# Kernel optimization log

Measured on AMD Instinct MI355X. Metric: run time of the kernel, lower is better.

The kernel has to match this reference:

```python
import jax, jax.numpy as jnp
import numpy as np

N_NODES = 100000
N_EDGES = 600000
N_GRAPHS = 2000
H = 128
L = 3
EPS = 1e-5


def layer_norm(x, g, b):
    m = jnp.mean(x, axis=-1, keepdims=True)
    v = jnp.mean((x - m) ** 2, axis=-1, keepdims=True)
    return (x - m) / jnp.sqrt(v + EPS) * g + b


def setup_inputs() -> dict:
    key = jax.random.key(0)
    ks = jax.random.split(key, 32)
    s = 0.05
    d = {}
    d['atom_features'] = jax.random.normal(ks[0], (N_NODES, 4), jnp.float32)
    d['edge_index'] = jax.random.randint(ks[1], (2, N_EDGES), 0, N_NODES, jnp.int32)
    d['edge_attr'] = jax.random.uniform(ks[2], (N_EDGES, 1), jnp.float32)
    d['batch'] = jnp.sort(jax.random.randint(ks[3], (N_NODES,), 0, N_GRAPHS, jnp.int32))
    # atom encoder
    d['enc_w'] = jax.random.normal(ks[4], (4, H)) * s
    d['enc_b'] = jnp.zeros((H,))
    d['enc_ln_g'] = jnp.ones((H,))
    d['enc_ln_b'] = jnp.zeros((H,))
    # stacked per-layer MPNN params (L layers)
    d['msg_w1'] = jax.random.normal(ks[5], (L, 2 * H + 1, 2 * H)) * s
    d['msg_b1'] = jnp.zeros((L, 2 * H))
    d['msg_w2'] = jax.random.normal(ks[6], (L, 2 * H, H)) * s
    d['msg_b2'] = jnp.zeros((L, H))
    d['gru_wih'] = jax.random.normal(ks[7], (L, 3 * H, H)) * s
    d['gru_whh'] = jax.random.normal(ks[8], (L, 3 * H, H)) * s
    d['gru_bih'] = jnp.zeros((L, 3 * H))
    d['gru_bhh'] = jnp.zeros((L, 3 * H))
    d['ln_g'] = jnp.ones((L, H))
    d['ln_b'] = jnp.zeros((L, H))
    # readout MLP (dropout is eval-mode identity)
    d['ro_w1'] = jax.random.normal(ks[9], (2 * H, H)) * s
    d['ro_b1'] = jnp.zeros((H,))
    d['ro_w2'] = jax.random.normal(ks[10], (H, H // 2)) * s
    d['ro_b2'] = jnp.zeros((H // 2,))
    d['ro_w3'] = jax.random.normal(ks[11], (H // 2, 113)) * s
    d['ro_b3'] = jnp.zeros((113,))
    return d


def _forward(atom_features, edge_attr, enc_w, enc_b, enc_ln_g, enc_ln_b,
             msg_w1, msg_b1, msg_w2, msg_b2, gru_wih, gru_whh, gru_bih, gru_bhh,
             ln_g, ln_b, ro_w1, ro_b1, ro_w2, ro_b2, ro_w3, ro_b3,
             edge_index, batch):
    n = atom_features.shape[0]
    x = layer_norm(jax.nn.relu(atom_features @ enc_w + enc_b), enc_ln_g, enc_ln_b)
    src, dst = edge_index[0], edge_index[1]
    for l in range(L):
        # gather-concat-MLP messages: [E, 2H+1] -> [E, 2H] -> [E, H]
        m = jnp.concatenate([x[src], x[dst], edge_attr], axis=-1)
        m = jax.nn.relu(m @ msg_w1[l] + msg_b1[l]) @ msg_w2[l] + msg_b2[l]
        aggr = jax.ops.segment_sum(m, dst, num_segments=n)  # index_add
        # GRUCell(input=aggr, hidden=x)
        gi = aggr @ gru_wih[l].T + gru_bih[l]
        gh = x @ gru_whh[l].T + gru_bhh[l]
        i_r, i_z, i_n = jnp.split(gi, 3, axis=-1)
        h_r, h_z, h_n = jnp.split(gh, 3, axis=-1)
        r = jax.nn.sigmoid(i_r + h_r)
        z = jax.nn.sigmoid(i_z + h_z)
        nn_ = jnp.tanh(i_n + r * h_n)
        x_new = (1.0 - z) * nn_ + z * x
        x = layer_norm(x + x_new, ln_g[l], ln_b[l])
    # per-graph mean+max pooling
    ones = jnp.ones((n,), x.dtype)
    counts = jax.ops.segment_sum(ones, batch, num_segments=N_GRAPHS)
    mean_pool = jax.ops.segment_sum(x, batch, num_segments=N_GRAPHS) / jnp.maximum(counts, 1.0)[:, None]
    max_pool = jax.ops.segment_max(x, batch, num_segments=N_GRAPHS)
    g = jnp.concatenate([mean_pool, max_pool], axis=-1)  # [B, 2H]
    h1 = jax.nn.relu(g @ ro_w1 + ro_b1)
    h2 = jax.nn.relu(h1 @ ro_w2 + ro_b2)
    return h2 @ ro_w3 + ro_b3  # [B, 113]


def reference(atom_features, edge_index, edge_attr, batch, enc_w, enc_b, enc_ln_g, enc_ln_b,
              msg_w1, msg_b1, msg_w2, msg_b2, gru_wih, gru_whh, gru_bih, gru_bhh,
              ln_g, ln_b, ro_w1, ro_b1, ro_w2, ro_b2, ro_w3, ro_b3):
    return _forward(atom_features, edge_attr, enc_w, enc_b, enc_ln_g, enc_ln_b,
                    msg_w1, msg_b1, msg_w2, msg_b2, gru_wih, gru_whh, gru_bih, gru_bhh,
                    ln_g, ln_b, ro_w1, ro_b1, ro_w2, ro_b2, ro_w3, ro_b3,
                    edge_index, batch)
```

## Files before the change

### kernel.cpp

```cpp
#include <hip/hip_runtime.h>
#include <hip/hip_bf16.h>
#include <math.h>

#define NN 100000
#define NE_TOT 600000
#define NG 2000
#define HD 128
#define NL 3
#define LN_EPS 1e-5f

typedef __attribute__((ext_vector_type(8))) short short8;
typedef __attribute__((ext_vector_type(4))) float f32x4;

__device__ __forceinline__ unsigned short f2bf(float f){
  union { float f; unsigned int u; } x; x.f = f;
  unsigned int r = (x.u + 0x7FFFu + ((x.u >> 16) & 1u)) >> 16;
  return (unsigned short)r;
}
__device__ __forceinline__ float bf2f(unsigned short u){
  union { unsigned int i; float f; } x; x.i = ((unsigned int)u) << 16; return x.f;
}

__device__ __forceinline__ float wave_sum64(float v){
  #pragma unroll
  for (int o = 32; o > 0; o >>= 1) v += __shfl_xor(v, o, 64);
  return v;
}

__global__ __launch_bounds__(256) void k_zero4(float4* p, int n4){
  int i = blockIdx.x * 256 + threadIdx.x;
  if (i < n4) p[i] = make_float4(0.f, 0.f, 0.f, 0.f);
}

__global__ __launch_bounds__(256) void k_hist(const int* __restrict__ ei, int* __restrict__ cnt){
  int e = blockIdx.x * 256 + threadIdx.x;
  if (e < NE_TOT) atomicAdd(&cnt[ei[NE_TOT + e]], 1);
}

__global__ __launch_bounds__(1024) void k_scan1(const int* __restrict__ cnt,
                                                int* __restrict__ loc,
                                                int* __restrict__ bsum){
  __shared__ int w_s[16];
  int t = threadIdx.x, lane = t & 63, wv = t >> 6;
  int g = blockIdx.x * 1024 + t;
  int v = (g < NN) ? cnt[g] : 0;
  int s = v;
  #pragma unroll
  for (int o = 1; o < 64; o <<= 1){
    int u = __shfl_up(s, o, 64);
    if (lane >= o) s += u;
  }
  if (lane == 63) w_s[wv] = s;
  __syncthreads();
  if (t == 0){
    int run = 0;
    #pragma unroll
    for (int i = 0; i < 16; ++i){ int c = w_s[i]; w_s[i] = run; run += c; }
    bsum[blockIdx.x] = run;
  }
  __syncthreads();
  if (g < NN) loc[g] = s - v + w_s[wv];
}

__global__ __launch_bounds__(128) void k_scan2(const int* __restrict__ bsum,
                                               int* __restrict__ bscan){
  __shared__ int w0_s;
  int t = threadIdx.x, lane = t & 63, wv = t >> 6;
  int v = (t < 98) ? bsum[t] : 0;
  int s = v;
  #pragma unroll
  for (int o = 1; o < 64; o <<= 1){
    int u = __shfl_up(s, o, 64);
    if (lane >= o) s += u;
  }
  if (wv == 0 && lane == 63) w0_s = s;
  __syncthreads();
  if (wv == 1) s += w0_s;
  if (t < 98) bscan[t] = s - v;
}

__global__ __launch_bounds__(1024) void k_scan3(const int* __restrict__ loc,
                                                const int* __restrict__ bscan,
                                                int* __restrict__ cur){
  int g = blockIdx.x * 1024 + threadIdx.x;
  if (g < NN) cur[g] = loc[g] + bscan[blockIdx.x];
}

__global__ __launch_bounds__(256) void k_scatter(const int* __restrict__ ei,
    const float* __restrict__ eattr, int* __restrict__ cur,
    int* __restrict__ srcs, int* __restrict__ dsts, float* __restrict__ attrs){
  int e = blockIdx.x * 256 + threadIdx.x;
  if (e >= NE_TOT) return;
  int d = ei[NE_TOT + e];
  int p = atomicAdd(&cur[d], 1);
  srcs[p] = ei[e];
  dsts[p] = d;
  attrs[p] = eattr[e];
}

#define GW_LPL 102400
#define GW_O2  67584
#define GW_O3  84992
__global__ __launch_bounds__(256) void k_gprep(const float* __restrict__ wih,
                                               const float* __restrict__ whh,
                                               unsigned short* __restrict__ gw){
  int idx = blockIdx.x * 256 + threadIdx.x;
  if (idx >= 2 * 3 * 384 * 128) return;
  int which = (idx >= 3 * 384 * 128);
  int i = which ? idx - 3 * 384 * 128 : idx;
  int l = i / 49152;
  int r = i - l * 49152;
  int j = r >> 7, k = r & 127;
  float v = which ? whh[i] : wih[i];
  size_t o;
  if (!which){
    o = (j < 256) ? ((size_t)l * GW_LPL + (size_t)j * 264 + k)
                  : ((size_t)l * GW_LPL + GW_O2 + (size_t)(j - 256) * 136 + k);
  } else {
    o = (j < 256) ? ((size_t)l * GW_LPL + (size_t)j * 264 + 128 + k)
                  : ((size_t)l * GW_LPL + GW_O3 + (size_t)(j - 256) * 136 + k);
  }
  gw[o] = f2bf(v);
}

#define W1N_LS (512 * 136)
__global__ __launch_bounds__(256) void k_mprep(const float* __restrict__ w1,
                                               unsigned short* __restrict__ w1n){
  int idx = blockIdx.x * 256 + threadIdx.x;
  if (idx >= 3 * 512 * 128) return;
  int l = idx / (512 * 128);
  int r = idx - l * (512 * 128);
  int j = r >> 7, k = r & 127;
  const float* wl = w1 + (size_t)l * 257 * 256;
  float v = (j < 256) ? wl[k * 256 + j] : wl[(128 + k) * 256 + (j - 256)];
  w1n[(size_t)l * W1N_LS + j * 136 + k] = f2bf(v);
}

#define W2T_LS (128 * 264)
__global__ __launch_bounds__(256) void k_w2prep(const float* __restrict__ w2,
                                                unsigned short* __restrict__ w2T){
  int idx = blockIdx.x * 256 + threadIdx.x;
  if (idx >= 3 * 128 * 256) return;
  int l = idx >> 15;
  int r = idx & 32767;
  int c = r >> 8, k = r & 255;
  w2T[(size_t)l * W2T_LS + c * 264 + k] = f2bf(w2[(size_t)l * 256 * 128 + k * 128 + c]);
}

__global__ __launch_bounds__(256) void k_enc(const float* __restrict__ af,
    const float* __restrict__ w, const float* __restrict__ b,
    const float* __restrict__ lg, const float* __restrict__ lb,
    unsigned short* __restrict__ xbf){
  int wv = threadIdx.x >> 6, lane = threadIdx.x & 63;
  int n = blockIdx.x * 4 + wv;
  float4 a = *reinterpret_cast<const float4*>(af + (size_t)n * 4);
  int c0 = lane, c1 = lane + 64;
  float v0 = fmaf(a.x, w[c0], fmaf(a.y, w[128 + c0], fmaf(a.z, w[256 + c0], fmaf(a.w, w[384 + c0], b[c0]))));
  float v1 = fmaf(a.x, w[c1], fmaf(a.y, w[128 + c1], fmaf(a.z, w[256 + c1], fmaf(a.w, w[384 + c1], b[c1]))));
  v0 = fmaxf(v0, 0.f); v1 = fmaxf(v1, 0.f);
  float m = wave_sum64(v0 + v1) * (1.f / 128.f);
  float d0 = v0 - m, d1 = v1 - m;
  float var = wave_sum64(d0 * d0 + d1 * d1) * (1.f / 128.f);
  float rstd = rsqrtf(var + LN_EPS);
  xbf[(size_t)n * HD + c0] = f2bf(d0 * rstd * lg[c0] + lb[c0]);
  xbf[(size_t)n * HD + c1] = f2bf(d1 * rstd * lg[c1] + lb[c1]);
}

__global__ __launch_bounds__(256, 2) void k_ngemm(const unsigned short* __restrict__ xbf,
    const unsigned short* __restrict__ w1n, const float* __restrict__ b1,
    unsigned short* __restrict__ gsd, float* __restrict__ aggr){
  int tid = threadIdx.x, lane = tid & 63, wv = tid >> 6;
  int r16 = lane & 15, kg = lane >> 4;
  {
    int nrow = NN - blockIdx.x * 64; if (nrow > 64) nrow = 64;
    float4* az = (float4*)(aggr + (size_t)blockIdx.x * 64 * HD);
    int n4 = nrow * (HD / 4);
    for (int i = tid; i < n4; i += 256) az[i] = make_float4(0.f, 0.f, 0.f, 0.f);
  }
  int n = blockIdx.x * 64 + wv * 16 + r16;
  int nc = (n < NN) ? n : NN - 1;
  short8 bfr[4];
  #pragma unroll
  for (int k0 = 0; k0 < 4; ++k0)
    bfr[k0] = *reinterpret_cast<const short8*>(xbf + (size_t)nc * HD + k0 * 32 + kg * 8);
  f32x4 acc[32];
  #pragma unroll
  for (int it = 0; it < 32; ++it) acc[it] = (f32x4){0.f, 0.f, 0.f, 0.f};
  #pragma unroll
  for (int it = 0; it < 32; ++it){
    const unsigned short* ap = w1n + (size_t)(it * 16 + r16) * 136 + kg * 8;
    #pragma unroll
    for (int k0 = 0; k0 < 4; ++k0){
      short8 af = *reinterpret_cast<const short8*>(ap + k0 * 32);
      acc[it] = __builtin_amdgcn_mfma_f32_16x16x32_bf16(af, bfr[k0], acc[it], 0, 0, 0);
    }
  }
  if (n < NN){
    #pragma unroll
    for (int it = 0; it < 32; ++it){
      int c0 = it * 16 + kg * 4;
      ushort4 h;
      float v0 = acc[it][0], v1 = acc[it][1], v2 = acc[it][2], v3 = acc[it][3];
      if (c0 >= 256){
        v0 += b1[c0 - 256]; v1 += b1[c0 - 255]; v2 += b1[c0 - 254]; v3 += b1[c0 - 253];
      }
      h.x = f2bf(v0); h.y = f2bf(v1); h.z = f2bf(v2); h.w = f2bf(v3);
      *reinterpret_cast<ushort4*>(gsd + (size_t)n * 512 + c0) = h;
    }
  }
}

#define EBM 64
__global__ __launch_bounds__(256, 4) void k_msg(const unsigned short* __restrict__ gsd,
    const int* __restrict__ srcs, const int* __restrict__ dsts,
    const float* __restrict__ attrs, const float* __restrict__ w1attr,
    const unsigned short* __restrict__ w2T, const float* __restrict__ b2,
    float* __restrict__ aggr){
  __shared__ __align__(16) unsigned char smem[33280];
  unsigned short* h_s = (unsigned short*)smem;
  float* scr = (float*)smem;
  __shared__ float w1a_s[256];
  __shared__ float b2_s[128];
  __shared__ int   dst_s[EBM];
  __shared__ float attr_s[EBM];
  int tid = threadIdx.x;
  int lane = tid & 63, wv = tid >> 6;
  int r16 = lane & 15, kg = lane >> 4;
  int ebase = blockIdx.x * EBM;

  w1a_s[tid] = w1attr[tid & 255];
  if (tid < 128) b2_s[tid] = b2[tid];
  if (tid < EBM){ dst_s[tid] = dsts[ebase + tid]; attr_s[tid] = attrs[ebase + tid]; }
  __syncthreads();

  {
    int e = tid >> 2, q = tid & 3;
    int sn = srcs[ebase + e];
    int dn = dst_s[e];
    float at = attr_s[e];
    const unsigned short* gp = gsd + (size_t)sn * 512;
    const unsigned short* dp = gsd + (size_t)dn * 512 + 256;
    short8 gv[8], dv[8];
    #pragma unroll
    for (int j8 = 0; j8 < 8; ++j8){
      int colb = j8 * 32 + q * 8;
      gv[j8] = *reinterpret_cast<const short8*>(gp + colb);
      dv[j8] = *reinterpret_cast<const short8*>(dp + colb);
    }
    __builtin_amdgcn_sched_barrier(0);
    #pragma unroll
    for (int j8 = 0; j8 < 8; ++j8){
      int colb = j8 * 32 + q * 8;
      unsigned short hh[8];
      #pragma unroll
      for (int i = 0; i < 8; ++i){
        float v = bf2f((unsigned short)gv[j8][i]) + bf2f((unsigned short)dv[j8][i]) + at * w1a_s[colb + i];
        hh[i] = f2bf(fmaxf(v, 0.f));
      }
      int slot = colb >> 3;
      int slotw = (slot & ~7) | ((slot ^ e) & 7);
      *reinterpret_cast<int4*>(&h_s[e * 256 + slotw * 8]) = *reinterpret_cast<int4*>(hh);
    }
  }
  __syncthreads();

  f32x4 acc2[4][2];
  #pragma unroll
  for (int rt = 0; rt < 4; ++rt)
    #pragma unroll
    for (int ct = 0; ct < 2; ++ct)
      acc2[rt][ct] = (f32x4){0.f, 0.f, 0.f, 0.f};
  int cbase2 = wv * 32;
  {
    short8 a[4], bb[2];
    const unsigned short* w2b = w2T + (size_t)(cbase2 + r16) * 264 + kg * 8;
    for (int k0 = 0; k0 < 8; ++k0){
      #pragma unroll
      for (int rt = 0; rt < 4; ++rt){
        int row = rt * 16 + r16;
        int slot = k0 * 4 + kg;
        int slotw = (slot & ~7) | ((slot ^ row) & 7);
        a[rt] = *reinterpret_cast<const short8*>(&h_s[row * 256 + slotw * 8]);
      }
      #pragma unroll
      for (int ct = 0; ct < 2; ++ct)
        bb[ct] = *reinterpret_cast<const short8*>(w2b + ct * 16 * 264 + k0 * 32);
      #pragma unroll
      for (int rt = 0; rt < 4; ++rt)
        #pragma unroll
        for (int ct = 0; ct < 2; ++ct)
          acc2[rt][ct] = __builtin_amdgcn_mfma_f32_16x16x32_bf16(a[rt], bb[ct], acc2[rt][ct], 0, 0, 0);
    }
  }
  __syncthreads();

  #pragma unroll
  for (int ct = 0; ct < 2; ++ct){
    int col = cbase2 + ct * 16 + r16;
    #pragma unroll
    for (int rt = 0; rt < 4; ++rt){
      #pragma unroll
      for (int r = 0; r < 4; ++r){
        int row = rt * 16 + kg * 4 + r;
        scr[row * 130 + col] = acc2[rt][ct][r];
      }
    }
  }
  __syncthreads();

  {
    int c = tid & 127, h = tid >> 7;
    int r0 = h * 32;
    float bias = b2_s[c];
    int pd = dst_s[r0];
    float acc = scr[r0 * 130 + c] + bias;
    #pragma unroll 4
    for (int r = 1; r < 32; ++r){
      int row = r0 + r;
      float v = scr[row * 130 + c] + bias;
      int d = dst_s[row];
      if (d != pd){
        atomicAdd(&aggr[(size_t)pd * HD + c], acc);
        acc = v; pd = d;
      } else {
        acc += v;
      }
    }
    atomicAdd(&aggr[(size_t)pd * HD + c], acc);
  }
}

#define GRB 64
__global__ __launch_bounds__(256, 2) void k_gru(unsigned short* __restrict__ xbf,
    const float* __restrict__ aggr,
    const unsigned short* __restrict__ gw,
    const float* __restrict__ bih, const float* __restrict__ bhh,
    const float* __restrict__ lg, const float* __restrict__ lb){
  __shared__ unsigned short a_s[GRB * 256];
  __shared__ float psum[GRB][2][2];
  int tid = threadIdx.x;
  int lane = tid & 63, wv = tid >> 6;
  int r16 = lane & 15, kg = lane >> 4;
  int rg = wv >> 1, cg = wv & 1;
  int nbase = blockIdx.x * GRB;

  {
    int row = tid >> 2, qc = (tid & 3) * 32;
    int n = nbase + row; if (n >= NN) n = NN - 1;
    const float* ap = aggr + (size_t)n * HD + qc;
    #pragma unroll
    for (int j = 0; j < 8; ++j){
      float4 v = *reinterpret_cast<const float4*>(ap + j * 4);
      ushort4 h;
      h.x = f2bf(v.x); h.y = f2bf(v.y); h.z = f2bf(v.z); h.w = f2bf(v.w);
      int col = qc + j * 4;
      int slot = col >> 3;
      int slotw = (slot & ~7) | ((slot ^ row) & 7);
      *reinterpret_cast<ushort4*>(&a_s[row * 256 + slotw * 8 + (col & 7)]) = h;
    }
  }
  {
    int row = tid >> 2, q = tid & 3;
    int n = nbase + row; if (n >= NN) n = NN - 1;
    const unsigned short* xp = xbf + (size_t)n * HD + q * 32;
    #pragma unroll
    for (int j = 0; j < 4; ++j){
      int4 v = *reinterpret_cast<const int4*>(xp + j * 8);
      int col = 128 + q * 32 + j * 8;
      int slot = col >> 3;
      int slotw = (slot & ~7) | ((slot ^ row) & 7);
      *reinterpret_cast<int4*>(&a_s[row * 256 + slotw * 8]) = v;
    }
  }
  __syncthreads();

  short8 a[2][8];
  #pragma unroll
  for (int rt = 0; rt < 2; ++rt){
    int arow = rg * 32 + rt * 16 + r16;
    #pragma unroll
    for (int k0 = 0; k0 < 8; ++k0){
      int slot = k0 * 4 + kg;
      int slotw = (slot & ~7) | ((slot ^ arow) & 7);
      a[rt][k0] = *reinterpret_cast<const short8*>(&a_s[arow * 256 + slotw * 8]);
    }
  }

  f32x4 accR[2][4], accZ[2][4], accI[2][4], accH[2][4];
  #pragma unroll
  for (int rt = 0; rt < 2; ++rt)
    #pragma unroll
    for (int ct = 0; ct < 4; ++ct){
      accR[rt][ct] = (f32x4){0.f, 0.f, 0.f, 0.f};
      accZ[rt][ct] = (f32x4){0.f, 0.f, 0.f, 0.f};
      accI[rt][ct] = (f32x4){0.f, 0.f, 0.f, 0.f};
      accH[rt][ct] = (f32x4){0.f, 0.f, 0.f, 0.f};
    }

  int jb = cg * 64;
  #pragma unroll
  for (int ct = 0; ct < 4; ++ct){
    const unsigned short* bpR = gw + (size_t)(jb + ct * 16 + r16) * 264 + kg * 8;
    const unsigned short* bpZ = gw + (size_t)(128 + jb + ct * 16 + r16) * 264 + kg * 8;
    #pragma unroll
    for (int k0 = 0; k0 < 8; ++k0){
      short8 bR = *reinterpret_cast<const short8*>(bpR + k0 * 32);
      accR[0][ct] = __builtin_amdgcn_mfma_f32_16x16x32_bf16(a[0][k0], bR, accR[0][ct], 0, 0, 0);
      accR[1][ct] = __builtin_amdgcn_mfma_f32_16x16x32_bf16(a[1][k0], bR, accR[1][ct], 0, 0, 0);
      short8 bZ = *reinterpret_cast<const short8*>(bpZ + k0 * 32);
      accZ[0][ct] = __builtin_amdgcn_mfma_f32_16x16x32_bf16(a[0][k0], bZ, accZ[0][ct], 0, 0, 0);
      accZ[1][ct] = __builtin_amdgcn_mfma_f32_16x16x32_bf16(a[1][k0], bZ, accZ[1][ct], 0, 0, 0);
    }
    const unsigned short* bpI = gw + GW_O2 + (size_t)(jb + ct * 16 + r16) * 136 + kg * 8;
    const unsigned short* bpH = gw + GW_O3 + (size_t)(jb + ct * 16 + r16) * 136 + kg * 8;
    #pragma unroll
    for (int k0 = 0; k0 < 4; ++k0){
      short8 bI = *reinterpret_cast<const short8*>(bpI + k0 * 32);
      accI[0][ct] = __builtin_amdgcn_mfma_f32_16x16x32_bf16(a[0][k0], bI, accI[0][ct], 0, 0, 0);
      accI[1][ct] = __builtin_amdgcn_mfma_f32_16x16x32_bf16(a[1][k0], bI, accI[1][ct], 0, 0, 0);
      short8 bH = *reinterpret_cast<const short8*>(bpH + k0 * 32);
      accH[0][ct] = __builtin_amdgcn_mfma_f32_16x16x32_bf16(a[0][k0 + 4], bH, accH[0][ct], 0, 0, 0);
      accH[1][ct] = __builtin_amdgcn_mfma_f32_16x16x32_bf16(a[1][k0 + 4], bH, accH[1][ct], 0, 0, 0);
    }
  }

  #pragma unroll
  for (int rt = 0; rt < 2; ++rt){
    #pragma unroll
    for (int ct = 0; ct < 4; ++ct){
      int j = jb + ct * 16 + r16;
      float br = bih[j] + bhh[j];
      float bz = bih[j + 128] + bhh[j + 128];
      float bin = bih[j + 256], bhn = bhh[j + 256];
      #pragma unroll
      for (int r = 0; r < 4; ++r){
        int n = nbase + rg * 32 + rt * 16 + kg * 4 + r;
        int nc = (n < NN) ? n : NN - 1;
        float xv = bf2f(xbf[(size_t)nc * HD + j]);
        float rgt = accR[rt][ct][r] + br;  rgt = 1.f / (1.f + __expf(-rgt));
        float zg  = accZ[rt][ct][r] + bz;  zg  = 1.f / (1.f + __expf(-zg));
        float ng  = tanhf(accI[rt][ct][r] + bin + rgt * (accH[rt][ct][r] + bhn));
        accR[rt][ct][r] = xv + (1.f - zg) * ng + zg * xv;
      }
    }
  }

  #pragma unroll
  for (int rt = 0; rt < 2; ++rt){
    #pragma unroll
    for (int r = 0; r < 4; ++r){
      float s = 0.f, q = 0.f;
      #pragma unroll
      for (int ct = 0; ct < 4; ++ct){ float v = accR[rt][ct][r]; s += v; q += v * v; }
      #pragma unroll
      for (int o = 1; o <= 8; o <<= 1){ s += __shfl_xor(s, o, 64); q += __shfl_xor(q, o, 64); }
      if (r16 == 0){
        int l = rg * 32 + rt * 16 + kg * 4 + r;
        psum[l][cg][0] = s;
        psum[l][cg][1] = q;
      }
    }
  }
  __syncthreads();

  #pragma unroll
  for (int rt = 0; rt < 2; ++rt){
    #pragma unroll
    for (int r = 0; r < 4; ++r){
      int l = rg * 32 + rt * 16 + kg * 4 + r;
      float S = psum[l][0][0] + psum[l][1][0];
      float Q = psum[l][0][1] + psum[l][1][1];
      float m = S * (1.f / 128.f);
      float var = Q * (1.f / 128.f) - m * m;
      float rstd = rsqrtf(fmaxf(var, 0.f) + LN_EPS);
      int n = nbase + rg * 32 + rt * 16 + kg * 4 + r;
      if (n < NN){
        #pragma unroll
        for (int ct = 0; ct < 4; ++ct){
          int j = jb + ct * 16 + r16;
          xbf[(size_t)n * HD + j] = f2bf((accR[rt][ct][r] - m) * rstd * lg[j] + lb[j]);
        }
      }
    }
  }
}

__device__ __forceinline__ int lowerb(const int* __restrict__ a, int v){
  int lo = 0, hi = NN;
  while (lo < hi){ int mid = (lo + hi) >> 1; if (a[mid] < v) lo = mid + 1; else hi = mid; }
  return lo;
}

__global__ __launch_bounds__(128) void k_pool(const unsigned short* __restrict__ xbf,
    const int* __restrict__ batch,
    const float* __restrict__ w1, const float* __restrict__ b1,
    const float* __restrict__ w2, const float* __restrict__ b2,
    const float* __restrict__ w3, const float* __restrict__ b3,
    float* __restrict__ out){
  __shared__ float g_s[256];
  __shared__ float h1_s[128];
  __shared__ float h2_s[64];
  int g = blockIdx.x, tid = threadIdx.x;
  int s = lowerb(batch, g), t = lowerb(batch, g + 1);
  float sum = 0.f, mx = -INFINITY;
  for (int n = s; n < t; ++n){
    float v = bf2f(xbf[(size_t)n * HD + tid]);
    sum += v; mx = fmaxf(mx, v);
  }
  int cnt = t - s;
  g_s[tid]       = sum / fmaxf((float)cnt, 1.f);
  g_s[tid + 128] = (cnt > 0) ? mx : -INFINITY;
  __syncthreads();
  float a1 = b1[tid];
  for (int k = 0; k < 256; ++k) a1 = fmaf(g_s[k], w1[k * 128 + tid], a1);
  h1_s[tid] = fmaxf(a1, 0.f);
  __syncthreads();
  if (tid < 64){
    float a2 = b2[tid];
    for (int k = 0; k < 128; ++k) a2 = fmaf(h1_s[k], w2[k * 64 + tid], a2);
    h2_s[tid] = fmaxf(a2, 0.f);
  }
  __syncthreads();
  if (tid < 113){
    float a3 = b3[tid];
    for (int k = 0; k < 64; ++k) a3 = fmaf(h2_s[k], w3[k * 113 + tid], a3);
    out[(size_t)g * 113 + tid] = a3;
  }
}

extern "C" void kernel_launch(void* const* d_in, const int* in_sizes, int n_in,
                              void* d_out, int out_size, void* d_ws, size_t ws_size,
                              hipStream_t stream){
  (void)in_sizes; (void)n_in; (void)out_size; (void)ws_size;
  const float* af     = (const float*)d_in[0];
  const int*   ei     = (const int*)  d_in[1];
  const float* eattr  = (const float*)d_in[2];
  const int*   batch  = (const int*)  d_in[3];
  const float* enc_w  = (const float*)d_in[4];
  const float* enc_b  = (const float*)d_in[5];
  const float* enc_lg = (const float*)d_in[6];
  const float* enc_lb = (const float*)d_in[7];
  const float* mw1    = (const float*)d_in[8];
  const float* mb1    = (const float*)d_in[9];
  const float* mw2    = (const float*)d_in[10];
  const float* mb2    = (const float*)d_in[11];
  const float* gwih   = (const float*)d_in[12];
  const float* gwhh   = (const float*)d_in[13];
  const float* gbih   = (const float*)d_in[14];
  const float* gbhh   = (const float*)d_in[15];
  const float* lng    = (const float*)d_in[16];
  const float* lnb    = (const float*)d_in[17];
  const float* rw1    = (const float*)d_in[18];
  const float* rb1    = (const float*)d_in[19];
  const float* rw2    = (const float*)d_in[20];
  const float* rb2    = (const float*)d_in[21];
  const float* rw3    = (const float*)d_in[22];
  const float* rb3    = (const float*)d_in[23];
  float* out = (float*)d_out;
  char* ws = (char*)d_ws;

  size_t off = 0;
  auto carve = [&](size_t bytes)->char*{
    char* p = ws + off;
    off = (off + bytes + 255) & ~(size_t)255;
    return p;
  };
  unsigned short* xbf  = (unsigned short*)carve((size_t)NN * HD * 2);
  float*          aggr = (float*)         carve((size_t)NN * HD * 4);
  unsigned short* gsd  = (unsigned short*)carve((size_t)NN * 512 * 2);
  unsigned short* gw   = (unsigned short*)carve((size_t)3 * GW_LPL * 2);
  unsigned short* w1n  = (unsigned short*)carve((size_t)3 * W1N_LS * 2);
  unsigned short* w2T  = (unsigned short*)carve((size_t)3 * W2T_LS * 2);
  int*   cnt   = (int*)  carve((size_t)NN * 4);
  int*   cur   = (int*)  carve((size_t)NN * 4);
  int*   loc   = (int*)  carve((size_t)NN * 4);
  int*   bsum  = (int*)  carve((size_t)128 * 4);
  int*   bscan = (int*)  carve((size_t)128 * 4);
  int*   srcs  = (int*)  carve((size_t)NE_TOT * 4);
  int*   dsts  = (int*)  carve((size_t)NE_TOT * 4);
  float* attrs = (float*)carve((size_t)NE_TOT * 4);

  k_zero4<<<(NN / 4 + 255) / 256, 256, 0, stream>>>((float4*)cnt, NN / 4);
  k_hist<<<(NE_TOT + 255) / 256, 256, 0, stream>>>(ei, cnt);
  k_scan1<<<98, 1024, 0, stream>>>(cnt, loc, bsum);
  k_scan2<<<1, 128, 0, stream>>>(bsum, bscan);
  k_scan3<<<98, 1024, 0, stream>>>(loc, bscan, cur);
  k_scatter<<<(NE_TOT + 255) / 256, 256, 0, stream>>>(ei, eattr, cur, srcs, dsts, attrs);
  k_gprep<<<1152, 256, 0, stream>>>(gwih, gwhh, gw);
  k_mprep<<<768, 256, 0, stream>>>(mw1, w1n);
  k_w2prep<<<384, 256, 0, stream>>>(mw2, w2T);
  k_enc<<<NN / 4, 256, 0, stream>>>(af, enc_w, enc_b, enc_lg, enc_lb, xbf);

  for (int l = 0; l < NL; ++l){
    k_ngemm<<<(NN + 63) / 64, 256, 0, stream>>>(xbf,
        w1n + (size_t)l * W1N_LS, mb1 + (size_t)l * 256, gsd, aggr);
    k_msg<<<NE_TOT / EBM, 256, 0, stream>>>(gsd, srcs, dsts, attrs,
        mw1 + (size_t)l * 257 * 256 + 256 * 256,
        w2T + (size_t)l * W2T_LS, mb2 + (size_t)l * 128, aggr);
    k_gru<<<(NN + GRB - 1) / GRB, 256, 0, stream>>>(xbf, aggr,
        gw + (size_t)l * GW_LPL,
        gbih + (size_t)l * 384, gbhh + (size_t)l * 384,
        lng + (size_t)l * HD, lnb + (size_t)l * HD);
  }
  k_pool<<<NG, 128, 0, stream>>>(xbf, batch, rw1, rb1, rw2, rb2, rw3, rb3, out);
}
```

Measured before the change: 1.002 ms.

## Fold message bias into aggr init, retile node GEMM, vectorize bf16 unpack, cheaper tanh

The second message-layer bias is no longer added per edge. It is folded into the aggregation buffer's initial value as in-degree times the bias, using the histogram counts computed earlier. The node GEMM is retiled so each wave covers 32 nodes by 256 output columns and reuses each weight fragment for two node tiles. The message kernel unpacks bf16 pairs from 32-bit words with shifts and masks, and the GRU uses a sigmoid-based tanh. Together these aim to cut per-edge ALU work and weight-load traffic, at the cost of a slight change in floating-point rounding and a tanh that loses accuracy at extreme inputs.

```diff
diff --git a/kernel.cpp b/kernel.cpp
--- a/kernel.cpp
+++ b/kernel.cpp
@@ -19,6 +19,12 @@
 }
 __device__ __forceinline__ float bf2f(unsigned short u){
   union { unsigned int i; float f; } x; x.i = ((unsigned int)u) << 16; return x.f;
+}
+__device__ __forceinline__ float asfloat_u(unsigned int u){
+  union { unsigned int i; float f; } x; x.i = u; return x.f;
+}
+__device__ __forceinline__ unsigned int pack_bf16x2(float lo, float hi){
+  return (unsigned int)f2bf(lo) | ((unsigned int)f2bf(hi) << 16);
 }
 
 __device__ __forceinline__ float wave_sum64(float v){
@@ -168,44 +174,62 @@
 
 __global__ __launch_bounds__(256, 2) void k_ngemm(const unsigned short* __restrict__ xbf,
     const unsigned short* __restrict__ w1n, const float* __restrict__ b1,
-    unsigned short* __restrict__ gsd, float* __restrict__ aggr){
+    unsigned short* __restrict__ gsd, float* __restrict__ aggr,
+    const int* __restrict__ cnt, const float* __restrict__ b2){
   int tid = threadIdx.x, lane = tid & 63, wv = tid >> 6;
   int r16 = lane & 15, kg = lane >> 4;
+  int rg = wv >> 1, cg = wv & 1;
   {
     int nrow = NN - blockIdx.x * 64; if (nrow > 64) nrow = 64;
-    float4* az = (float4*)(aggr + (size_t)blockIdx.x * 64 * HD);
-    int n4 = nrow * (HD / 4);
-    for (int i = tid; i < n4; i += 256) az[i] = make_float4(0.f, 0.f, 0.f, 0.f);
-  }
-  int n = blockIdx.x * 64 + wv * 16 + r16;
-  int nc = (n < NN) ? n : NN - 1;
-  short8 bfr[4];
-  #pragma unroll
-  for (int k0 = 0; k0 < 4; ++k0)
-    bfr[k0] = *reinterpret_cast<const short8*>(xbf + (size_t)nc * HD + k0 * 32 + kg * 8);
-  f32x4 acc[32];
-  #pragma unroll
-  for (int it = 0; it < 32; ++it) acc[it] = (f32x4){0.f, 0.f, 0.f, 0.f};
-  #pragma unroll
-  for (int it = 0; it < 32; ++it){
-    const unsigned short* ap = w1n + (size_t)(it * 16 + r16) * 136 + kg * 8;
+    for (int i = tid; i < nrow * 32; i += 256){
+      int row = i >> 5, c4 = (i & 31) * 4;
+      int n = blockIdx.x * 64 + row;
+      float cv = (float)cnt[n];
+      float4 bb = *reinterpret_cast<const float4*>(b2 + c4);
+      bb.x *= cv; bb.y *= cv; bb.z *= cv; bb.w *= cv;
+      *reinterpret_cast<float4*>(aggr + (size_t)n * HD + c4) = bb;
+    }
+  }
+  int n0 = blockIdx.x * 64 + rg * 32 + r16;
+  int n1 = n0 + 16;
+  int nc0 = (n0 < NN) ? n0 : NN - 1;
+  int nc1 = (n1 < NN) ? n1 : NN - 1;
+  short8 bfr[2][4];
+  #pragma unroll
+  for (int k0 = 0; k0 < 4; ++k0){
+    bfr[0][k0] = *reinterpret_cast<const short8*>(xbf + (size_t)nc0 * HD + k0 * 32 + kg * 8);
+    bfr[1][k0] = *reinterpret_cast<const short8*>(xbf + (size_t)nc1 * HD + k0 * 32 + kg * 8);
+  }
+  f32x4 acc[2][16];
+  #pragma unroll
+  for (int nt = 0; nt < 2; ++nt)
+    #pragma unroll
+    for (int it = 0; it < 16; ++it) acc[nt][it] = (f32x4){0.f, 0.f, 0.f, 0.f};
+  #pragma unroll
+  for (int it = 0; it < 16; ++it){
+    const unsigned short* ap = w1n + (size_t)(cg * 256 + it * 16 + r16) * 136 + kg * 8;
     #pragma unroll
     for (int k0 = 0; k0 < 4; ++k0){
       short8 af = *reinterpret_cast<const short8*>(ap + k0 * 32);
-      acc[it] = __builtin_amdgcn_mfma_f32_16x16x32_bf16(af, bfr[k0], acc[it], 0, 0, 0);
-    }
-  }
-  if (n < NN){
-    #pragma unroll
-    for (int it = 0; it < 32; ++it){
-      int c0 = it * 16 + kg * 4;
-      ushort4 h;
-      float v0 = acc[it][0], v1 = acc[it][1], v2 = acc[it][2], v3 = acc[it][3];
-      if (c0 >= 256){
-        v0 += b1[c0 - 256]; v1 += b1[c0 - 255]; v2 += b1[c0 - 254]; v3 += b1[c0 - 253];
-      }
-      h.x = f2bf(v0); h.y = f2bf(v1); h.z = f2bf(v2); h.w = f2bf(v3);
-      *reinterpret_cast<ushort4*>(gsd + (size_t)n * 512 + c0) = h;
+      acc[0][it] = __builtin_amdgcn_mfma_f32_16x16x32_bf16(af, bfr[0][k0], acc[0][it], 0, 0, 0);
+      acc[1][it] = __builtin_amdgcn_mfma_f32_16x16x32_bf16(af, bfr[1][k0], acc[1][it], 0, 0, 0);
+    }
+  }
+  #pragma unroll
+  for (int nt = 0; nt < 2; ++nt){
+    int n = blockIdx.x * 64 + rg * 32 + nt * 16 + r16;
+    if (n < NN){
+      #pragma unroll
+      for (int it = 0; it < 16; ++it){
+        int co = it * 16 + kg * 4;
+        float v0 = acc[nt][it][0], v1 = acc[nt][it][1], v2 = acc[nt][it][2], v3 = acc[nt][it][3];
+        if (cg){
+          v0 += b1[co]; v1 += b1[co + 1]; v2 += b1[co + 2]; v3 += b1[co + 3];
+        }
+        ushort4 h;
+        h.x = f2bf(v0); h.y = f2bf(v1); h.z = f2bf(v2); h.w = f2bf(v3);
+        *reinterpret_cast<ushort4*>(gsd + (size_t)n * 512 + cg * 256 + co) = h;
+      }
     }
   }
 }
@@ -214,13 +238,12 @@
 __global__ __launch_bounds__(256, 4) void k_msg(const unsigned short* __restrict__ gsd,
     const int* __restrict__ srcs, const int* __restrict__ dsts,
     const float* __restrict__ attrs, const float* __restrict__ w1attr,
-    const unsigned short* __restrict__ w2T, const float* __restrict__ b2,
+    const unsigned short* __restrict__ w2T,
     float* __restrict__ aggr){
   __shared__ __align__(16) unsigned char smem[33280];
   unsigned short* h_s = (unsigned short*)smem;
   float* scr = (float*)smem;
   __shared__ float w1a_s[256];
-  __shared__ float b2_s[128];
   __shared__ int   dst_s[EBM];
   __shared__ float attr_s[EBM];
   int tid = threadIdx.x;
@@ -229,7 +252,6 @@
   int ebase = blockIdx.x * EBM;
 
   w1a_s[tid] = w1attr[tid & 255];
-  if (tid < 128) b2_s[tid] = b2[tid];
   if (tid < EBM){ dst_s[tid] = dsts[ebase + tid]; attr_s[tid] = attrs[ebase + tid]; }
   __syncthreads();
 
@@ -238,28 +260,33 @@
     int sn = srcs[ebase + e];
     int dn = dst_s[e];
     float at = attr_s[e];
-    const unsigned short* gp = gsd + (size_t)sn * 512;
-    const unsigned short* dp = gsd + (size_t)dn * 512 + 256;
-    short8 gv[8], dv[8];
+    const uint4* gp = reinterpret_cast<const uint4*>(gsd + (size_t)sn * 512);
+    const uint4* dp = reinterpret_cast<const uint4*>(gsd + (size_t)dn * 512 + 256);
+    uint4 gv[8], dv[8];
+    #pragma unroll
+    for (int j8 = 0; j8 < 8; ++j8){
+      gv[j8] = gp[j8 * 4 + q];
+      dv[j8] = dp[j8 * 4 + q];
+    }
+    __builtin_amdgcn_sched_barrier(0);
     #pragma unroll
     for (int j8 = 0; j8 < 8; ++j8){
       int colb = j8 * 32 + q * 8;
-      gv[j8] = *reinterpret_cast<const short8*>(gp + colb);
-      dv[j8] = *reinterpret_cast<const short8*>(dp + colb);
-    }
-    __builtin_amdgcn_sched_barrier(0);
-    #pragma unroll
-    for (int j8 = 0; j8 < 8; ++j8){
-      int colb = j8 * 32 + q * 8;
-      unsigned short hh[8];
-      #pragma unroll
-      for (int i = 0; i < 8; ++i){
-        float v = bf2f((unsigned short)gv[j8][i]) + bf2f((unsigned short)dv[j8][i]) + at * w1a_s[colb + i];
-        hh[i] = f2bf(fmaxf(v, 0.f));
+      unsigned int hh[4];
+      unsigned int ug[4] = {gv[j8].x, gv[j8].y, gv[j8].z, gv[j8].w};
+      unsigned int ud[4] = {dv[j8].x, dv[j8].y, dv[j8].z, dv[j8].w};
+      #pragma unroll
+      for (int w = 0; w < 4; ++w){
+        float glo = asfloat_u(ug[w] << 16), ghi = asfloat_u(ug[w] & 0xFFFF0000u);
+        float dlo = asfloat_u(ud[w] << 16), dhi = asfloat_u(ud[w] & 0xFFFF0000u);
+        float vlo = fmaxf(glo + dlo + at * w1a_s[colb + 2 * w],     0.f);
+        float vhi = fmaxf(ghi + dhi + at * w1a_s[colb + 2 * w + 1], 0.f);
+        hh[w] = pack_bf16x2(vlo, vhi);
       }
       int slot = colb >> 3;
       int slotw = (slot & ~7) | ((slot ^ e) & 7);
-      *reinterpret_cast<int4*>(&h_s[e * 256 + slotw * 8]) = *reinterpret_cast<int4*>(hh);
+      *reinterpret_cast<uint4*>(&h_s[e * 256 + slotw * 8]) =
+          make_uint4(hh[0], hh[1], hh[2], hh[3]);
     }
   }
   __syncthreads();
@@ -311,13 +338,12 @@
   {
     int c = tid & 127, h = tid >> 7;
     int r0 = h * 32;
-    float bias = b2_s[c];
     int pd = dst_s[r0];
-    float acc = scr[r0 * 130 + c] + bias;
+    float acc = scr[r0 * 130 + c];
     #pragma unroll 4
     for (int r = 1; r < 32; ++r){
       int row = r0 + r;
-      float v = scr[row * 130 + c] + bias;
+      float v = scr[row * 130 + c];
       int d = dst_s[row];
       if (d != pd){
         atomicAdd(&aggr[(size_t)pd * HD + c], acc);
@@ -439,7 +465,9 @@
         float xv = bf2f(xbf[(size_t)nc * HD + j]);
         float rgt = accR[rt][ct][r] + br;  rgt = 1.f / (1.f + __expf(-rgt));
         float zg  = accZ[rt][ct][r] + bz;  zg  = 1.f / (1.f + __expf(-zg));
-        float ng  = tanhf(accI[rt][ct][r] + bin + rgt * (accH[rt][ct][r] + bhn));
+        float na  = accI[rt][ct][r] + bin + rgt * (accH[rt][ct][r] + bhn);
+        float sg  = 1.f / (1.f + __expf(-2.f * na));
+        float ng  = fmaf(2.f, sg, -1.f);
         accR[rt][ct][r] = xv + (1.f - zg) * ng + zg * xv;
       }
     }
@@ -593,10 +621,11 @@
 
   for (int l = 0; l < NL; ++l){
     k_ngemm<<<(NN + 63) / 64, 256, 0, stream>>>(xbf,
-        w1n + (size_t)l * W1N_LS, mb1 + (size_t)l * 256, gsd, aggr);
+        w1n + (size_t)l * W1N_LS, mb1 + (size_t)l * 256, gsd, aggr,
+        cnt, mb2 + (size_t)l * 128);
     k_msg<<<NE_TOT / EBM, 256, 0, stream>>>(gsd, srcs, dsts, attrs,
         mw1 + (size_t)l * 257 * 256 + 256 * 256,
-        w2T + (size_t)l * W2T_LS, mb2 + (size_t)l * 128, aggr);
+        w2T + (size_t)l * W2T_LS, aggr);
     k_gru<<<(NN + GRB - 1) / GRB, 256, 0, stream>>>(xbf, aggr,
         gw + (size_t)l * GW_LPL,
         gbih + (size_t)l * 384, gbhh + (size_t)l * 384,
```

Measured after the change: 955.7 us. -4.6%, faster.
